# Kernel tuning notes

Hardware: AMD Instinct MI355X
Metric: run time of the kernel (lower is better)

## Reference

```python
import jax, jax.numpy as jnp
import numpy as np

REG = 0.1          # entropic regularization, as in the module
N_ITERS = 100      # fixed Sinkhorn iteration count (POT numItermax capped; see notes)


def _sqdist(x, y):
    # ot.dist default: squared Euclidean pairwise distances, [n, m]
    x2 = jnp.sum(x * x, axis=1)[:, None]
    y2 = jnp.sum(y * y, axis=1)[None, :]
    M = x2 + y2 - 2.0 * (x @ y.T)
    return jnp.maximum(M, 0.0)


def setup_inputs() -> dict:
    key = jax.random.key(0)
    kx, ky = jax.random.split(key)
    n, m, d = 4096, 4096, 32
    # uniform in [0, 0.5) keeps exp(-M/reg) representable in fp32
    x = jax.random.uniform(kx, (n, d), dtype=jnp.float32) * 0.5
    y = jax.random.uniform(ky, (m, d), dtype=jnp.float32) * 0.5
    return {"x": x, "y": y}


def reference(x, y):
    n, m = x.shape[0], y.shape[0]
    a = jnp.full((n,), 1.0 / n, dtype=x.dtype)   # uniform source marginal
    b = jnp.full((m,), 1.0 / m, dtype=y.dtype)   # uniform target marginal
    M = _sqdist(x, y)                            # [n, m] cost
    K = jnp.exp(-M / REG)                        # [n, m] Gibbs kernel

    u0 = jnp.full((n,), 1.0 / n, dtype=x.dtype)
    v0 = jnp.full((m,), 1.0 / m, dtype=y.dtype)

    def step(carry, _):
        u, v = carry
        u = a / (K @ v)      # [n]
        v = b / (K.T @ u)    # [m]
        return (u, v), None

    (u, v), _ = jax.lax.scan(step, (u0, v0), None, length=N_ITERS)
    # transport plan gamma = diag(u) K diag(v), as returned by ot.bregman.sinkhorn
    gamma = u[:, None] * K * v[None, :]
    return gamma
```

## Files before the change

kernel.cpp:

```cpp
#include <hip/hip_runtime.h>
#include <hip/hip_fp16.h>


#define NN 4096
#define MM 4096
#define DD 32
#define N_ITERS 100

static constexpr float INV_REG = 10.0f;
static constexpr float A_MARG  = 1.0f / 4096.0f;
static constexpr float B_MARG  = 1.0f / 4096.0f;

typedef _Float16 h2_t __attribute__((ext_vector_type(2)));
typedef unsigned u32v4 __attribute__((ext_vector_type(4)));

static __device__ __forceinline__ float dot2(unsigned a, unsigned b, float acc) {
#if __has_builtin(__builtin_amdgcn_fdot2)
    return __builtin_amdgcn_fdot2(__builtin_bit_cast(h2_t, a),
                                  __builtin_bit_cast(h2_t, b), acc, false);
#else
    float2 fa = __half22float2(*(const __half2*)&a);
    float2 fb = __half22float2(*(const __half2*)&b);
    acc = fmaf(fa.x, fb.x, acc);
    return fmaf(fa.y, fb.y, acc);
#endif
}

static __device__ __forceinline__ uint4 ld_nt_u4(const uint4* p) {
#if __has_builtin(__builtin_nontemporal_load)
    u32v4 r = __builtin_nontemporal_load((const u32v4*)p);
    uint4 o; o.x = r[0]; o.y = r[1]; o.z = r[2]; o.w = r[3];
    return o;
#else
    return *p;
#endif
}

static __device__ __forceinline__ unsigned ld_dev_u32(const unsigned* p) {
    return __hip_atomic_load(p, __ATOMIC_RELAXED, __HIP_MEMORY_SCOPE_AGENT);
}
static __device__ __forceinline__ void st_dev_u32(unsigned* p, unsigned v) {
    __hip_atomic_store(p, v, __ATOMIC_RELAXED, __HIP_MEMORY_SCOPE_AGENT);
}
static __device__ __forceinline__ unsigned short ld_dev_u16(const unsigned short* p) {
    return __hip_atomic_load(p, __ATOMIC_RELAXED, __HIP_MEMORY_SCOPE_AGENT);
}
static __device__ __forceinline__ void st_dev_u16(unsigned short* p, unsigned short v) {
    __hip_atomic_store(p, v, __ATOMIC_RELAXED, __HIP_MEMORY_SCOPE_AGENT);
}
static __device__ __forceinline__ unsigned long long ld_dev_u64(const unsigned long long* p) {
    return __hip_atomic_load(p, __ATOMIC_RELAXED, __HIP_MEMORY_SCOPE_AGENT);
}
static __device__ __forceinline__ void st_dev_u64(unsigned long long* p, unsigned long long v) {
    __hip_atomic_store(p, v, __ATOMIC_RELAXED, __HIP_MEMORY_SCOPE_AGENT);
}

__global__ void compute_K_half(const float* __restrict__ p, const float* __restrict__ q,
                               __half* __restrict__ Kh, __half* __restrict__ v16,
                               unsigned* __restrict__ conv, unsigned* __restrict__ slot,
                               unsigned* __restrict__ mtu, unsigned* __restrict__ mtv,
                               int prime) {
    const int tid = threadIdx.x;
    const int j   = blockIdx.x * 256 + tid;
    const int r0  = blockIdx.y * 16;

    if (prime && blockIdx.y == 0) {
        v16[j] = __float2half(B_MARG);
        if (blockIdx.x == 0) {
            if (tid == 0) { *conv = 0u; *slot = 1u; }
            mtu[tid] = 0u; mtu[tid + 256] = 0u;
            mtv[tid] = 0u; mtv[tid + 256] = 0u;
        }
    }

    float qv[DD];
    const float4* q4 = (const float4*)(q + (size_t)j * DD);
#pragma unroll
    for (int k = 0; k < DD / 4; ++k) {
        float4 t = q4[k];
        qv[4 * k + 0] = t.x; qv[4 * k + 1] = t.y;
        qv[4 * k + 2] = t.z; qv[4 * k + 3] = t.w;
    }

    __shared__ float ps[16 * DD];
    ps[tid]       = p[(size_t)r0 * DD + tid];
    ps[tid + 256] = p[(size_t)r0 * DD + tid + 256];
    __syncthreads();

#pragma unroll 4
    for (int ii = 0; ii < 16; ++ii) {
        float acc = 0.0f;
#pragma unroll
        for (int k = 0; k < DD; ++k) {
            float d = ps[ii * DD + k] - qv[k];
            acc = fmaf(d, d, acc);
        }
        Kh[(size_t)(r0 + ii) * MM + j] = __float2half(__expf(-acc * INV_REG));
    }
}

__global__ void __launch_bounds__(1024, 8)
sinkhorn_persist(const __half* __restrict__ Kh, const __half* __restrict__ KTh,
                 float* __restrict__ u32g, float* __restrict__ v32g,
                 unsigned short* __restrict__ hist,
                 unsigned* __restrict__ mtu, unsigned* __restrict__ mtv,
                 unsigned long long* __restrict__ mdu,
                 unsigned long long* __restrict__ mdv) {
    __shared__ __align__(16) __half vlds[MM];
    __shared__ float part[16];
    __shared__ unsigned fb_lds[8];
    const int tid  = threadIdx.x;
    const int lane = tid & 63;
    const int w    = tid >> 6;
    const int rib  = w >> 1;
    const int hlf  = w & 1;
    const int bid  = blockIdx.x;
    const int i    = bid * 8 + rib;
    const int g0   = hlf * 256 + lane;
    const uint4* __restrict__ MU = (const uint4*)(Kh  + (size_t)i * MM);
    const uint4* __restrict__ MV = (const uint4*)(KTh + (size_t)i * MM);

    uint4 k0 = MU[g0], k1 = MU[g0 + 64], k2 = MU[g0 + 128], k3 = MU[g0 + 192];

    for (int t = 0; t < N_ITERS; ++t) {
        if (t == 0) {
            if (tid < 512) {
                const unsigned long long dv =
                    (unsigned long long)__half_as_ushort(__float2half(B_MARG)) *
                    0x0001000100010001ULL;
                ((unsigned long long*)vlds)[2 * tid]     = dv;
                ((unsigned long long*)vlds)[2 * tid + 1] = dv;
            }
            __syncthreads();
        } else {
            if (tid < 512) {
                const unsigned want = 2u * (unsigned)t;
                unsigned tg;
                for (;;) {
                    tg = ld_dev_u32(mtv + tid);
                    if ((tg & 0x7fffffffu) == want) break;
                    __builtin_amdgcn_s_sleep(1);
                }
                asm volatile("" ::: "memory");
                unsigned long long d0 = ld_dev_u64(mdv + 2 * tid);
                unsigned long long d1 = ld_dev_u64(mdv + 2 * tid + 1);
                ((unsigned long long*)vlds)[2 * tid]     = d0;
                ((unsigned long long*)vlds)[2 * tid + 1] = d1;
                const bool allf = __all((tg >> 31) != 0u);
                if ((tid & 63) == 0) fb_lds[tid >> 6] = allf ? 1u : 0u;
            }
            __syncthreads();
            if ((t & 1) == 0) {
                if ((fb_lds[0] & fb_lds[1] & fb_lds[2] & fb_lds[3] &
                     fb_lds[4] & fb_lds[5] & fb_lds[6] & fb_lds[7]) != 0u)
                    break;
            }
        }

        {
            const uint4* V = (const uint4*)vlds;
            const uint4 a = V[g0], b = V[g0 + 64], c = V[g0 + 128], d = V[g0 + 192];
            float x0 = 0.f, x1 = 0.f, x2 = 0.f, x3 = 0.f;
            x0 = dot2(k0.x, a.x, x0); x0 = dot2(k0.y, a.y, x0);
            x0 = dot2(k0.z, a.z, x0); x0 = dot2(k0.w, a.w, x0);
            x1 = dot2(k1.x, b.x, x1); x1 = dot2(k1.y, b.y, x1);
            x1 = dot2(k1.z, b.z, x1); x1 = dot2(k1.w, b.w, x1);
            x2 = dot2(k2.x, c.x, x2); x2 = dot2(k2.y, c.y, x2);
            x2 = dot2(k2.z, c.z, x2); x2 = dot2(k2.w, c.w, x2);
            x3 = dot2(k3.x, d.x, x3); x3 = dot2(k3.y, d.y, x3);
            x3 = dot2(k3.z, d.z, x3); x3 = dot2(k3.w, d.w, x3);
            float acc = (x0 + x1) + (x2 + x3);
#pragma unroll
            for (int off = 32; off > 0; off >>= 1) acc += __shfl_down(acc, off, 64);
            if (lane == 0) part[w] = acc;
        }
        if (w != 0) {
            k0 = ld_nt_u4(MV + g0);       k1 = ld_nt_u4(MV + g0 + 64);
            k2 = ld_nt_u4(MV + g0 + 128); k3 = ld_nt_u4(MV + g0 + 192);
        }
        __syncthreads();
        if (tid == 0) {
            unsigned long long d0 = 0, d1 = 0;
#pragma unroll
            for (int q = 0; q < 8; ++q) {
                float r = A_MARG / (part[2 * q] + part[2 * q + 1]);
                u32g[bid * 8 + q] = r;
                const unsigned long long h =
                    (unsigned long long)__half_as_ushort(__float2half(r));
                if (q < 4) d0 |= h << (16 * q); else d1 |= h << (16 * (q - 4));
            }
            st_dev_u64(mdu + 2 * bid,     d0);
            st_dev_u64(mdu + 2 * bid + 1, d1);
            asm volatile("s_waitcnt vmcnt(0)" ::: "memory");
            st_dev_u32(mtu + bid, 2u * (unsigned)t + 1u);
        }
        if (w == 0) {
            k0 = ld_nt_u4(MV + g0);       k1 = ld_nt_u4(MV + g0 + 64);
            k2 = ld_nt_u4(MV + g0 + 128); k3 = ld_nt_u4(MV + g0 + 192);
        }

        if (tid < 512) {
            const unsigned want = 2u * (unsigned)t + 1u;
            unsigned tg;
            for (;;) {
                tg = ld_dev_u32(mtu + tid);
                if ((tg & 0x7fffffffu) == want) break;
                __builtin_amdgcn_s_sleep(1);
            }
            asm volatile("" ::: "memory");
            unsigned long long d0 = ld_dev_u64(mdu + 2 * tid);
            unsigned long long d1 = ld_dev_u64(mdu + 2 * tid + 1);
            ((unsigned long long*)vlds)[2 * tid]     = d0;
            ((unsigned long long*)vlds)[2 * tid + 1] = d1;
        }
        __syncthreads();

        {
            const uint4* V = (const uint4*)vlds;
            const uint4 a = V[g0], b = V[g0 + 64], c = V[g0 + 128], d = V[g0 + 192];
            float x0 = 0.f, x1 = 0.f, x2 = 0.f, x3 = 0.f;
            x0 = dot2(k0.x, a.x, x0); x0 = dot2(k0.y, a.y, x0);
            x0 = dot2(k0.z, a.z, x0); x0 = dot2(k0.w, a.w, x0);
            x1 = dot2(k1.x, b.x, x1); x1 = dot2(k1.y, b.y, x1);
            x1 = dot2(k1.z, b.z, x1); x1 = dot2(k1.w, b.w, x1);
            x2 = dot2(k2.x, c.x, x2); x2 = dot2(k2.y, c.y, x2);
            x2 = dot2(k2.z, c.z, x2); x2 = dot2(k2.w, c.w, x2);
            x3 = dot2(k3.x, d.x, x3); x3 = dot2(k3.y, d.y, x3);
            x3 = dot2(k3.z, d.z, x3); x3 = dot2(k3.w, d.w, x3);
            float acc = (x0 + x1) + (x2 + x3);
#pragma unroll
            for (int off = 32; off > 0; off >>= 1) acc += __shfl_down(acc, off, 64);
            if (lane == 0) part[w] = acc;
        }
        if (w != 0) {
            k0 = MU[g0]; k1 = MU[g0 + 64]; k2 = MU[g0 + 128]; k3 = MU[g0 + 192];
        }
        __syncthreads();
        if (tid == 0) {
            unsigned long long d0 = 0, d1 = 0;
#pragma unroll
            for (int q = 0; q < 8; ++q) {
                float r = B_MARG / (part[2 * q] + part[2 * q + 1]);
                v32g[bid * 8 + q] = r;
                const unsigned long long h =
                    (unsigned long long)__half_as_ushort(__float2half(r));
                if (q < 4) d0 |= h << (16 * q); else d1 |= h << (16 * (q - 4));
            }
            unsigned tg = 2u * (unsigned)t + 2u;
            if (t & 1) {
                unsigned long long h0 = ld_dev_u64((unsigned long long*)hist + 2 * bid);
                unsigned long long h1 = ld_dev_u64((unsigned long long*)hist + 2 * bid + 1);
                if (h0 == d0 && h1 == d1) tg |= 0x80000000u;
                st_dev_u64((unsigned long long*)hist + 2 * bid,     d0);
                st_dev_u64((unsigned long long*)hist + 2 * bid + 1, d1);
            }
            st_dev_u64(mdv + 2 * bid,     d0);
            st_dev_u64(mdv + 2 * bid + 1, d1);
            asm volatile("s_waitcnt vmcnt(0)" ::: "memory");
            st_dev_u32(mtv + bid, tg);
        }
        if (w == 0) {
            k0 = MU[g0]; k1 = MU[g0 + 64]; k2 = MU[g0 + 128]; k3 = MU[g0 + 192];
        }
    }
}

__global__ void __launch_bounds__(1024, 8)
rowpass_u(const __half* __restrict__ Mat, const __half* __restrict__ w16_in,
          float* __restrict__ w32_out, __half* __restrict__ w16_out,
          unsigned* __restrict__ conv, unsigned* __restrict__ slot, int t) {
    if (ld_dev_u32(conv)) return;
    if ((t & 1) == 0) {
        if (ld_dev_u32(slot) == 0u) {
            if (threadIdx.x == 0) st_dev_u32(conv, 1u);
            return;
        }
    } else {
        if (blockIdx.x == 0 && threadIdx.x == 0) st_dev_u32(slot, 0u);
    }

    __shared__ __align__(16) __half vlds[MM];
    __shared__ float part[16];
    const int tid  = threadIdx.x;
    const int lane = tid & 63;
    const int w    = tid >> 6;
    const int rib  = w >> 1;
    const int hlf  = w & 1;
    const int i    = blockIdx.x * 8 + rib;
    const uint4* __restrict__ Mrow = (const uint4*)(Mat + (size_t)i * MM);
    const int g0 = hlf * 256 + lane;

    uint4 stg;
    if (tid < 512) stg = ((const uint4*)w16_in)[tid];
    const uint4 k0 = Mrow[g0];
    const uint4 k1 = Mrow[g0 + 64];
    const uint4 k2 = Mrow[g0 + 128];
    const uint4 k3 = Mrow[g0 + 192];
    if (tid < 512) ((uint4*)vlds)[tid] = stg;
    __syncthreads();

    const uint4* V = (const uint4*)vlds;
    const uint4 v0 = V[g0];
    const uint4 v1 = V[g0 + 64];
    const uint4 v2 = V[g0 + 128];
    const uint4 v3 = V[g0 + 192];

    float a0 = 0.f, a1 = 0.f, a2 = 0.f, a3 = 0.f;
    a0 = dot2(k0.x, v0.x, a0); a0 = dot2(k0.y, v0.y, a0);
    a0 = dot2(k0.z, v0.z, a0); a0 = dot2(k0.w, v0.w, a0);
    a1 = dot2(k1.x, v1.x, a1); a1 = dot2(k1.y, v1.y, a1);
    a1 = dot2(k1.z, v1.z, a1); a1 = dot2(k1.w, v1.w, a1);
    a2 = dot2(k2.x, v2.x, a2); a2 = dot2(k2.y, v2.y, a2);
    a2 = dot2(k2.z, v2.z, a2); a2 = dot2(k2.w, v2.w, a2);
    a3 = dot2(k3.x, v3.x, a3); a3 = dot2(k3.y, v3.y, a3);
    a3 = dot2(k3.z, v3.z, a3); a3 = dot2(k3.w, v3.w, a3);
    float acc = (a0 + a1) + (a2 + a3);

#pragma unroll
    for (int off = 32; off > 0; off >>= 1) acc += __shfl_down(acc, off, 64);
    if (lane == 0) part[w] = acc;
    __syncthreads();

    if (tid < 8) {
        const int row = blockIdx.x * 8 + tid;
        float r = A_MARG / (part[2 * tid] + part[2 * tid + 1]);
        w32_out[row] = r;
        w16_out[row] = __float2half(r);
    }
}

__global__ void __launch_bounds__(1024, 8)
rowpass_v(const __half* __restrict__ Mat, const __half* __restrict__ w16_in,
          float* __restrict__ w32_out, __half* __restrict__ w16_out,
          unsigned short* __restrict__ hist,
          unsigned* __restrict__ conv, unsigned* __restrict__ slot, int t) {
    if (ld_dev_u32(conv)) return;

    __shared__ __align__(16) __half vlds[MM];
    __shared__ float part[16];
    const int tid  = threadIdx.x;
    const int lane = tid & 63;
    const int w    = tid >> 6;
    const int rib  = w >> 1;
    const int hlf  = w & 1;
    const int i    = blockIdx.x * 8 + rib;
    const uint4* __restrict__ Mrow = (const uint4*)(Mat + (size_t)i * MM);
    const int g0 = hlf * 256 + lane;

    uint4 stg;
    if (tid < 512) stg = ((const uint4*)w16_in)[tid];
    const uint4 k0 = Mrow[g0];
    const uint4 k1 = Mrow[g0 + 64];
    const uint4 k2 = Mrow[g0 + 128];
    const uint4 k3 = Mrow[g0 + 192];
    if (tid < 512) ((uint4*)vlds)[tid] = stg;
    __syncthreads();

    const uint4* V = (const uint4*)vlds;
    const uint4 v0 = V[g0];
    const uint4 v1 = V[g0 + 64];
    const uint4 v2 = V[g0 + 128];
    const uint4 v3 = V[g0 + 192];

    float a0 = 0.f, a1 = 0.f, a2 = 0.f, a3 = 0.f;
    a0 = dot2(k0.x, v0.x, a0); a0 = dot2(k0.y, v0.y, a0);
    a0 = dot2(k0.z, v0.z, a0); a0 = dot2(k0.w, v0.w, a0);
    a1 = dot2(k1.x, v1.x, a1); a1 = dot2(k1.y, v1.y, a1);
    a1 = dot2(k1.z, v1.z, a1); a1 = dot2(k1.w, v1.w, a1);
    a2 = dot2(k2.x, v2.x, a2); a2 = dot2(k2.y, v2.y, a2);
    a2 = dot2(k2.z, v2.z, a2); a2 = dot2(k2.w, v2.w, a2);
    a3 = dot2(k3.x, v3.x, a3); a3 = dot2(k3.y, v3.y, a3);
    a3 = dot2(k3.z, v3.z, a3); a3 = dot2(k3.w, v3.w, a3);
    float acc = (a0 + a1) + (a2 + a3);

#pragma unroll
    for (int off = 32; off > 0; off >>= 1) acc += __shfl_down(acc, off, 64);
    if (lane == 0) part[w] = acc;
    __syncthreads();

    if (tid < 8) {
        const int row = blockIdx.x * 8 + tid;
        float r = B_MARG / (part[2 * tid] + part[2 * tid + 1]);
        w32_out[row] = r;
        const __half h = __float2half(r);
        if (t & 1) {
            const unsigned short bits = __half_as_ushort(h);
            const unsigned short old2 = ld_dev_u16(hist + row);
            if (old2 != bits) st_dev_u32(slot, 1u);
            st_dev_u16(hist + row, bits);
        }
        w16_out[row] = h;
    }
}

__global__ void epilogue(const float* __restrict__ x, const float* __restrict__ y,
                         const float* __restrict__ u, const float* __restrict__ v,
                         float* __restrict__ out) {
    const int tid = threadIdx.x;
    const int j   = blockIdx.x * 256 + tid;
    const int r0  = blockIdx.y * 16;

    float yv[DD];
    const float4* y4 = (const float4*)(y + (size_t)j * DD);
#pragma unroll
    for (int k = 0; k < DD / 4; ++k) {
        float4 t = y4[k];
        yv[4 * k + 0] = t.x; yv[4 * k + 1] = t.y;
        yv[4 * k + 2] = t.z; yv[4 * k + 3] = t.w;
    }

    __shared__ float xs[16 * DD];
    __shared__ float u_lds[16];
    xs[tid]       = x[(size_t)r0 * DD + tid];
    xs[tid + 256] = x[(size_t)r0 * DD + tid + 256];
    if (tid < 16) u_lds[tid] = u[r0 + tid];
    __syncthreads();

    const float vj = v[j];
#pragma unroll 4
    for (int ii = 0; ii < 16; ++ii) {
        float acc = 0.0f;
#pragma unroll
        for (int k = 0; k < DD; ++k) {
            float d = xs[ii * DD + k] - yv[k];
            acc = fmaf(d, d, acc);
        }
        out[(size_t)(r0 + ii) * MM + j] = u_lds[ii] * __expf(-acc * INV_REG) * vj;
    }
}

extern "C" void kernel_launch(void* const* d_in, const int* in_sizes, int n_in,
                              void* d_out, int out_size, void* d_ws, size_t ws_size,
                              hipStream_t stream) {
    const float* x = (const float*)d_in[0];
    const float* y = (const float*)d_in[1];
    __half*   Kh   = (__half*)d_ws;
    __half*   KTh  = Kh + (size_t)NN * MM;
    float*    u32  = (float*)(KTh + (size_t)NN * MM);
    float*    v32  = u32 + NN;
    __half*   u16  = (__half*)(v32 + MM);
    __half*   v16  = u16 + NN;
    unsigned short* hist = (unsigned short*)(v16 + MM);
    unsigned* slot = (unsigned*)(hist + MM);
    unsigned* conv = slot + 1;
    unsigned* mtu  = slot + 512;
    unsigned* mtv  = mtu + 512;
    unsigned long long* mdu = (unsigned long long*)(mtv + 512);
    unsigned long long* mdv = mdu + 1024;
    float*    out  = (float*)d_out;

    compute_K_half<<<dim3(MM / 256, NN / 16), 256, 0, stream>>>(x, y, Kh, v16, conv, slot, mtu, mtv, 1);
    compute_K_half<<<dim3(NN / 256, MM / 16), 256, 0, stream>>>(y, x, KTh, v16, conv, slot, mtu, mtv, 0);

    {
        void* args[] = { &Kh, &KTh, &u32, &v32, &hist, &mtu, &mtv, &mdu, &mdv };
        hipError_t e = hipLaunchCooperativeKernel((const void*)sinkhorn_persist,
                                                  dim3(512), dim3(1024), args, 0, stream);
        if (e != hipSuccess) {
            (void)hipGetLastError();
            for (int t = 0; t < N_ITERS; ++t) {
                rowpass_u<<<NN / 8, 1024, 0, stream>>>(Kh,  v16, u32, u16, conv, slot, t);
                rowpass_v<<<MM / 8, 1024, 0, stream>>>(KTh, u16, v32, v16, hist, conv, slot, t);
            }
        }
    }

    epilogue<<<dim3(MM / 256, NN / 16), 256, 0, stream>>>(x, y, u32, v32, out);
}
```

Baseline: 621.4 us.

## Load broadcast vectors directly into registers per wave, drop LDS staging barriers

```diff
diff --git a/kernel.cpp b/kernel.cpp
--- a/kernel.cpp
+++ b/kernel.cpp
@@ -55,6 +55,15 @@
     __hip_atomic_store(p, v, __ATOMIC_RELAXED, __HIP_MEMORY_SCOPE_AGENT);
 }
 
+static __device__ __forceinline__ uint4 ld_ent(const unsigned long long* md, int e) {
+    unsigned long long d0 = ld_dev_u64(md + 2 * e);
+    unsigned long long d1 = ld_dev_u64(md + 2 * e + 1);
+    uint4 r;
+    r.x = (unsigned)d0; r.y = (unsigned)(d0 >> 32);
+    r.z = (unsigned)d1; r.w = (unsigned)(d1 >> 32);
+    return r;
+}
+
 __global__ void compute_K_half(const float* __restrict__ p, const float* __restrict__ q,
                                __half* __restrict__ Kh, __half* __restrict__ v16,
                                unsigned* __restrict__ conv, unsigned* __restrict__ slot,
@@ -102,13 +111,11 @@
 __global__ void __launch_bounds__(1024, 8)
 sinkhorn_persist(const __half* __restrict__ Kh, const __half* __restrict__ KTh,
                  float* __restrict__ u32g, float* __restrict__ v32g,
-                 unsigned short* __restrict__ hist,
                  unsigned* __restrict__ mtu, unsigned* __restrict__ mtv,
                  unsigned long long* __restrict__ mdu,
                  unsigned long long* __restrict__ mdv) {
-    __shared__ __align__(16) __half vlds[MM];
     __shared__ float part[16];
-    __shared__ unsigned fb_lds[8];
+    __shared__ unsigned fb_lds[16];
     const int tid  = threadIdx.x;
     const int lane = tid & 63;
     const int w    = tid >> 6;
@@ -117,58 +124,48 @@
     const int bid  = blockIdx.x;
     const int i    = bid * 8 + rib;
     const int g0   = hlf * 256 + lane;
+    const int e0 = g0, e1 = g0 + 64, e2 = g0 + 128, e3 = g0 + 192;
     const uint4* __restrict__ MU = (const uint4*)(Kh  + (size_t)i * MM);
     const uint4* __restrict__ MV = (const uint4*)(KTh + (size_t)i * MM);
 
+    unsigned long long h0p = ~0ULL, h1p = ~0ULL;
+
     uint4 k0 = MU[g0], k1 = MU[g0 + 64], k2 = MU[g0 + 128], k3 = MU[g0 + 192];
 
     for (int t = 0; t < N_ITERS; ++t) {
+        uint4 va, vb, vc, vd;
         if (t == 0) {
-            if (tid < 512) {
-                const unsigned long long dv =
-                    (unsigned long long)__half_as_ushort(__float2half(B_MARG)) *
-                    0x0001000100010001ULL;
-                ((unsigned long long*)vlds)[2 * tid]     = dv;
-                ((unsigned long long*)vlds)[2 * tid + 1] = dv;
-            }
-            __syncthreads();
+            const unsigned dv2 =
+                0x00010001u * (unsigned)__half_as_ushort(__float2half(B_MARG));
+            va.x = va.y = va.z = va.w = dv2; vb = va; vc = va; vd = va;
         } else {
-            if (tid < 512) {
-                const unsigned want = 2u * (unsigned)t;
-                unsigned tg;
-                for (;;) {
-                    tg = ld_dev_u32(mtv + tid);
-                    if ((tg & 0x7fffffffu) == want) break;
-                    __builtin_amdgcn_s_sleep(1);
-                }
-                asm volatile("" ::: "memory");
-                unsigned long long d0 = ld_dev_u64(mdv + 2 * tid);
-                unsigned long long d1 = ld_dev_u64(mdv + 2 * tid + 1);
-                ((unsigned long long*)vlds)[2 * tid]     = d0;
-                ((unsigned long long*)vlds)[2 * tid + 1] = d1;
-                const bool allf = __all((tg >> 31) != 0u);
-                if ((tid & 63) == 0) fb_lds[tid >> 6] = allf ? 1u : 0u;
-            }
-            __syncthreads();
-            if ((t & 1) == 0) {
-                if ((fb_lds[0] & fb_lds[1] & fb_lds[2] & fb_lds[3] &
-                     fb_lds[4] & fb_lds[5] & fb_lds[6] & fb_lds[7]) != 0u)
+            const unsigned want = 2u * (unsigned)t;
+            unsigned t0, t1, t2, t3;
+            for (;;) {
+                t0 = ld_dev_u32(mtv + e0); t1 = ld_dev_u32(mtv + e1);
+                t2 = ld_dev_u32(mtv + e2); t3 = ld_dev_u32(mtv + e3);
+                if (((t0 & 0x7fffffffu) == want) && ((t1 & 0x7fffffffu) == want) &&
+                    ((t2 & 0x7fffffffu) == want) && ((t3 & 0x7fffffffu) == want))
                     break;
-            }
+                __builtin_amdgcn_s_sleep(1);
+            }
+            asm volatile("" ::: "memory");
+            va = ld_ent(mdv, e0); vb = ld_ent(mdv, e1);
+            vc = ld_ent(mdv, e2); vd = ld_ent(mdv, e3);
+            const bool fz = __all(((t0 & t1 & t2 & t3) >> 31) != 0u);
+            if (lane == 0) fb_lds[w] = fz ? 1u : 0u;
         }
 
         {
-            const uint4* V = (const uint4*)vlds;
-            const uint4 a = V[g0], b = V[g0 + 64], c = V[g0 + 128], d = V[g0 + 192];
             float x0 = 0.f, x1 = 0.f, x2 = 0.f, x3 = 0.f;
-            x0 = dot2(k0.x, a.x, x0); x0 = dot2(k0.y, a.y, x0);
-            x0 = dot2(k0.z, a.z, x0); x0 = dot2(k0.w, a.w, x0);
-            x1 = dot2(k1.x, b.x, x1); x1 = dot2(k1.y, b.y, x1);
-            x1 = dot2(k1.z, b.z, x1); x1 = dot2(k1.w, b.w, x1);
-            x2 = dot2(k2.x, c.x, x2); x2 = dot2(k2.y, c.y, x2);
-            x2 = dot2(k2.z, c.z, x2); x2 = dot2(k2.w, c.w, x2);
-            x3 = dot2(k3.x, d.x, x3); x3 = dot2(k3.y, d.y, x3);
-            x3 = dot2(k3.z, d.z, x3); x3 = dot2(k3.w, d.w, x3);
+            x0 = dot2(k0.x, va.x, x0); x0 = dot2(k0.y, va.y, x0);
+            x0 = dot2(k0.z, va.z, x0); x0 = dot2(k0.w, va.w, x0);
+            x1 = dot2(k1.x, vb.x, x1); x1 = dot2(k1.y, vb.y, x1);
+            x1 = dot2(k1.z, vb.z, x1); x1 = dot2(k1.w, vb.w, x1);
+            x2 = dot2(k2.x, vc.x, x2); x2 = dot2(k2.y, vc.y, x2);
+            x2 = dot2(k2.z, vc.z, x2); x2 = dot2(k2.w, vc.w, x2);
+            x3 = dot2(k3.x, vd.x, x3); x3 = dot2(k3.y, vd.y, x3);
+            x3 = dot2(k3.z, vd.z, x3); x3 = dot2(k3.w, vd.w, x3);
             float acc = (x0 + x1) + (x2 + x3);
 #pragma unroll
             for (int off = 32; off > 0; off >>= 1) acc += __shfl_down(acc, off, 64);
@@ -179,54 +176,67 @@
             k2 = ld_nt_u4(MV + g0 + 128); k3 = ld_nt_u4(MV + g0 + 192);
         }
         __syncthreads();
-        if (tid == 0) {
-            unsigned long long d0 = 0, d1 = 0;
-#pragma unroll
-            for (int q = 0; q < 8; ++q) {
-                float r = A_MARG / (part[2 * q] + part[2 * q + 1]);
-                u32g[bid * 8 + q] = r;
-                const unsigned long long h =
-                    (unsigned long long)__half_as_ushort(__float2half(r));
-                if (q < 4) d0 |= h << (16 * q); else d1 |= h << (16 * (q - 4));
-            }
-            st_dev_u64(mdu + 2 * bid,     d0);
-            st_dev_u64(mdu + 2 * bid + 1, d1);
-            asm volatile("s_waitcnt vmcnt(0)" ::: "memory");
-            st_dev_u32(mtu + bid, 2u * (unsigned)t + 1u);
+        if (t != 0 && (t & 1) == 0) {
+            unsigned f = 1u;
+#pragma unroll
+            for (int q = 0; q < 16; ++q) f &= fb_lds[q];
+            if (f) break;
+        }
+        if (w == 0) {
+            unsigned hb = 0u;
+            if (lane < 8) {
+                float r = A_MARG / (part[2 * lane] + part[2 * lane + 1]);
+                u32g[bid * 8 + lane] = r;
+                hb = (unsigned)__half_as_ushort(__float2half(r));
+            }
+            const unsigned q0 = __shfl(hb, 0, 64), q1 = __shfl(hb, 1, 64);
+            const unsigned q2 = __shfl(hb, 2, 64), q3 = __shfl(hb, 3, 64);
+            const unsigned q4 = __shfl(hb, 4, 64), q5 = __shfl(hb, 5, 64);
+            const unsigned q6 = __shfl(hb, 6, 64), q7 = __shfl(hb, 7, 64);
+            if (lane == 0) {
+                const unsigned long long d0 =
+                    (unsigned long long)(q0 | (q1 << 16)) |
+                    ((unsigned long long)(q2 | (q3 << 16)) << 32);
+                const unsigned long long d1 =
+                    (unsigned long long)(q4 | (q5 << 16)) |
+                    ((unsigned long long)(q6 | (q7 << 16)) << 32);
+                st_dev_u64(mdu + 2 * bid,     d0);
+                st_dev_u64(mdu + 2 * bid + 1, d1);
+                asm volatile("s_waitcnt vmcnt(0)" ::: "memory");
+                st_dev_u32(mtu + bid, 2u * (unsigned)t + 1u);
+            }
         }
         if (w == 0) {
             k0 = ld_nt_u4(MV + g0);       k1 = ld_nt_u4(MV + g0 + 64);
             k2 = ld_nt_u4(MV + g0 + 128); k3 = ld_nt_u4(MV + g0 + 192);
         }
 
-        if (tid < 512) {
+        {
             const unsigned want = 2u * (unsigned)t + 1u;
-            unsigned tg;
+            unsigned t0, t1, t2, t3;
             for (;;) {
-                tg = ld_dev_u32(mtu + tid);
-                if ((tg & 0x7fffffffu) == want) break;
+                t0 = ld_dev_u32(mtu + e0); t1 = ld_dev_u32(mtu + e1);
+                t2 = ld_dev_u32(mtu + e2); t3 = ld_dev_u32(mtu + e3);
+                if (((t0 & 0x7fffffffu) == want) && ((t1 & 0x7fffffffu) == want) &&
+                    ((t2 & 0x7fffffffu) == want) && ((t3 & 0x7fffffffu) == want))
+                    break;
                 __builtin_amdgcn_s_sleep(1);
             }
             asm volatile("" ::: "memory");
-            unsigned long long d0 = ld_dev_u64(mdu + 2 * tid);
-            unsigned long long d1 = ld_dev_u64(mdu + 2 * tid + 1);
-            ((unsigned long long*)vlds)[2 * tid]     = d0;
-            ((unsigned long long*)vlds)[2 * tid + 1] = d1;
-        }
-        __syncthreads();
+            va = ld_ent(mdu, e0); vb = ld_ent(mdu, e1);
+            vc = ld_ent(mdu, e2); vd = ld_ent(mdu, e3);
+        }
 
         {
-            const uint4* V = (const uint4*)vlds;
-            const uint4 a = V[g0], b = V[g0 + 64], c = V[g0 + 128], d = V[g0 + 192];
             float x0 = 0.f, x1 = 0.f, x2 = 0.f, x3 = 0.f;
-            x0 = dot2(k0.x, a.x, x0); x0 = dot2(k0.y, a.y, x0);
-            x0 = dot2(k0.z, a.z, x0); x0 = dot2(k0.w, a.w, x0);
-            x1 = dot2(k1.x, b.x, x1); x1 = dot2(k1.y, b.y, x1);
-            x1 = dot2(k1.z, b.z, x1); x1 = dot2(k1.w, b.w, x1);
-            x2 = dot2(k2.x, c.x, x2); x2 = dot2(k2.y, c.y, x2);
-            x2 = dot2(k2.z, c.z, x2); x2 = dot2(k2.w, c.w, x2);
-            x3 = dot2(k3.x, d.x, x3); x3 = dot2(k3.y, d.y, x3);
-            x3 = dot2(k3.z, d.z, x3); x3 = dot2(k3.w, d.w, x3);
+            x0 = dot2(k0.x, va.x, x0); x0 = dot2(k0.y, va.y, x0);
+            x0 = dot2(k0.z, va.z, x0); x0 = dot2(k0.w, va.w, x0);
+            x1 = dot2(k1.x, vb.x, x1); x1 = dot2(k1.y, vb.y, x1);
+            x1 = dot2(k1.z, vb.z, x1); x1 = dot2(k1.w, vb.w, x1);
+            x2 = dot2(k2.x, vc.x, x2); x2 = dot2(k2.y, vc.y, x2);
+            x2 = dot2(k2.z, vc.z, x2); x2 = dot2(k2.w, vc.w, x2);
+            x3 = dot2(k3.x, vd.x, x3); x3 = dot2(k3.y, vd.y, x3);
+            x3 = dot2(k3.z, vd.z, x3); x3 = dot2(k3.w, vd.w, x3);
             float acc = (x0 + x1) + (x2 + x3);
 #pragma unroll
             for (int off = 32; off > 0; off >>= 1) acc += __shfl_down(acc, off, 64);
@@ -236,28 +246,34 @@
             k0 = MU[g0]; k1 = MU[g0 + 64]; k2 = MU[g0 + 128]; k3 = MU[g0 + 192];
         }
         __syncthreads();
-        if (tid == 0) {
-            unsigned long long d0 = 0, d1 = 0;
-#pragma unroll
-            for (int q = 0; q < 8; ++q) {
-                float r = B_MARG / (part[2 * q] + part[2 * q + 1]);
-                v32g[bid * 8 + q] = r;
-                const unsigned long long h =
-                    (unsigned long long)__half_as_ushort(__float2half(r));
-                if (q < 4) d0 |= h << (16 * q); else d1 |= h << (16 * (q - 4));
-            }
-            unsigned tg = 2u * (unsigned)t + 2u;
-            if (t & 1) {
-                unsigned long long h0 = ld_dev_u64((unsigned long long*)hist + 2 * bid);
-                unsigned long long h1 = ld_dev_u64((unsigned long long*)hist + 2 * bid + 1);
-                if (h0 == d0 && h1 == d1) tg |= 0x80000000u;
-                st_dev_u64((unsigned long long*)hist + 2 * bid,     d0);
-                st_dev_u64((unsigned long long*)hist + 2 * bid + 1, d1);
-            }
-            st_dev_u64(mdv + 2 * bid,     d0);
-            st_dev_u64(mdv + 2 * bid + 1, d1);
-            asm volatile("s_waitcnt vmcnt(0)" ::: "memory");
-            st_dev_u32(mtv + bid, tg);
+        if (w == 0) {
+            unsigned hb = 0u;
+            if (lane < 8) {
+                float r = B_MARG / (part[2 * lane] + part[2 * lane + 1]);
+                v32g[bid * 8 + lane] = r;
+                hb = (unsigned)__half_as_ushort(__float2half(r));
+            }
+            const unsigned q0 = __shfl(hb, 0, 64), q1 = __shfl(hb, 1, 64);
+            const unsigned q2 = __shfl(hb, 2, 64), q3 = __shfl(hb, 3, 64);
+            const unsigned q4 = __shfl(hb, 4, 64), q5 = __shfl(hb, 5, 64);
+            const unsigned q6 = __shfl(hb, 6, 64), q7 = __shfl(hb, 7, 64);
+            if (lane == 0) {
+                const unsigned long long d0 =
+                    (unsigned long long)(q0 | (q1 << 16)) |
+                    ((unsigned long long)(q2 | (q3 << 16)) << 32);
+                const unsigned long long d1 =
+                    (unsigned long long)(q4 | (q5 << 16)) |
+                    ((unsigned long long)(q6 | (q7 << 16)) << 32);
+                unsigned tg = 2u * (unsigned)t + 2u;
+                if (t & 1) {
+                    if (d0 == h0p && d1 == h1p) tg |= 0x80000000u;
+                    h0p = d0; h1p = d1;
+                }
+                st_dev_u64(mdv + 2 * bid,     d0);
+                st_dev_u64(mdv + 2 * bid + 1, d1);
+                asm volatile("s_waitcnt vmcnt(0)" ::: "memory");
+                st_dev_u32(mtv + bid, tg);
+            }
         }
         if (w == 0) {
             k0 = MU[g0]; k1 = MU[g0 + 64]; k2 = MU[g0 + 128]; k3 = MU[g0 + 192];
@@ -453,7 +469,7 @@
     compute_K_half<<<dim3(NN / 256, MM / 16), 256, 0, stream>>>(y, x, KTh, v16, conv, slot, mtu, mtv, 0);
 
     {
-        void* args[] = { &Kh, &KTh, &u32, &v32, &hist, &mtu, &mtv, &mdu, &mdv };
+        void* args[] = { &Kh, &KTh, &u32, &v32, &mtu, &mtv, &mdu, &mdv };
         hipError_t e = hipLaunchCooperativeKernel((const void*)sinkhorn_persist,
                                                   dim3(512), dim3(1024), args, 0, stream);
         if (e != hipSuccess) {
```

Measured after the change: 1.016 ms. 63.6% more time.

## Keep both K and K^T row slices resident in registers across Sinkhorn iterations

Applied to the files above, without the earlier changes.

```diff
diff --git a/kernel.cpp b/kernel.cpp
--- a/kernel.cpp
+++ b/kernel.cpp
@@ -12,7 +12,6 @@
 static constexpr float B_MARG  = 1.0f / 4096.0f;
 
 typedef _Float16 h2_t __attribute__((ext_vector_type(2)));
-typedef unsigned u32v4 __attribute__((ext_vector_type(4)));
 
 static __device__ __forceinline__ float dot2(unsigned a, unsigned b, float acc) {
 #if __has_builtin(__builtin_amdgcn_fdot2)
@@ -26,16 +25,6 @@
 #endif
 }
 
-static __device__ __forceinline__ uint4 ld_nt_u4(const uint4* p) {
-#if __has_builtin(__builtin_nontemporal_load)
-    u32v4 r = __builtin_nontemporal_load((const u32v4*)p);
-    uint4 o; o.x = r[0]; o.y = r[1]; o.z = r[2]; o.w = r[3];
-    return o;
-#else
-    return *p;
-#endif
-}
-
 static __device__ __forceinline__ unsigned ld_dev_u32(const unsigned* p) {
     return __hip_atomic_load(p, __ATOMIC_RELAXED, __HIP_MEMORY_SCOPE_AGENT);
 }
@@ -102,7 +91,6 @@
 __global__ void __launch_bounds__(1024, 8)
 sinkhorn_persist(const __half* __restrict__ Kh, const __half* __restrict__ KTh,
                  float* __restrict__ u32g, float* __restrict__ v32g,
-                 unsigned short* __restrict__ hist,
                  unsigned* __restrict__ mtu, unsigned* __restrict__ mtv,
                  unsigned long long* __restrict__ mdu,
                  unsigned long long* __restrict__ mdv) {
@@ -120,7 +108,10 @@
     const uint4* __restrict__ MU = (const uint4*)(Kh  + (size_t)i * MM);
     const uint4* __restrict__ MV = (const uint4*)(KTh + (size_t)i * MM);
 
-    uint4 k0 = MU[g0], k1 = MU[g0 + 64], k2 = MU[g0 + 128], k3 = MU[g0 + 192];
+    const uint4 ku0 = MU[g0], ku1 = MU[g0 + 64], ku2 = MU[g0 + 128], ku3 = MU[g0 + 192];
+    const uint4 kv0 = MV[g0], kv1 = MV[g0 + 64], kv2 = MV[g0 + 128], kv3 = MV[g0 + 192];
+
+    unsigned long long h0p = ~0ULL, h1p = ~0ULL;
 
     for (int t = 0; t < N_ITERS; ++t) {
         if (t == 0) {
@@ -161,42 +152,43 @@
             const uint4* V = (const uint4*)vlds;
             const uint4 a = V[g0], b = V[g0 + 64], c = V[g0 + 128], d = V[g0 + 192];
             float x0 = 0.f, x1 = 0.f, x2 = 0.f, x3 = 0.f;
-            x0 = dot2(k0.x, a.x, x0); x0 = dot2(k0.y, a.y, x0);
-            x0 = dot2(k0.z, a.z, x0); x0 = dot2(k0.w, a.w, x0);
-            x1 = dot2(k1.x, b.x, x1); x1 = dot2(k1.y, b.y, x1);
-            x1 = dot2(k1.z, b.z, x1); x1 = dot2(k1.w, b.w, x1);
-            x2 = dot2(k2.x, c.x, x2); x2 = dot2(k2.y, c.y, x2);
-            x2 = dot2(k2.z, c.z, x2); x2 = dot2(k2.w, c.w, x2);
-            x3 = dot2(k3.x, d.x, x3); x3 = dot2(k3.y, d.y, x3);
-            x3 = dot2(k3.z, d.z, x3); x3 = dot2(k3.w, d.w, x3);
+            x0 = dot2(ku0.x, a.x, x0); x0 = dot2(ku0.y, a.y, x0);
+            x0 = dot2(ku0.z, a.z, x0); x0 = dot2(ku0.w, a.w, x0);
+            x1 = dot2(ku1.x, b.x, x1); x1 = dot2(ku1.y, b.y, x1);
+            x1 = dot2(ku1.z, b.z, x1); x1 = dot2(ku1.w, b.w, x1);
+            x2 = dot2(ku2.x, c.x, x2); x2 = dot2(ku2.y, c.y, x2);
+            x2 = dot2(ku2.z, c.z, x2); x2 = dot2(ku2.w, c.w, x2);
+            x3 = dot2(ku3.x, d.x, x3); x3 = dot2(ku3.y, d.y, x3);
+            x3 = dot2(ku3.z, d.z, x3); x3 = dot2(ku3.w, d.w, x3);
             float acc = (x0 + x1) + (x2 + x3);
 #pragma unroll
             for (int off = 32; off > 0; off >>= 1) acc += __shfl_down(acc, off, 64);
             if (lane == 0) part[w] = acc;
         }
-        if (w != 0) {
-            k0 = ld_nt_u4(MV + g0);       k1 = ld_nt_u4(MV + g0 + 64);
-            k2 = ld_nt_u4(MV + g0 + 128); k3 = ld_nt_u4(MV + g0 + 192);
-        }
         __syncthreads();
-        if (tid == 0) {
-            unsigned long long d0 = 0, d1 = 0;
-#pragma unroll
-            for (int q = 0; q < 8; ++q) {
-                float r = A_MARG / (part[2 * q] + part[2 * q + 1]);
-                u32g[bid * 8 + q] = r;
-                const unsigned long long h =
-                    (unsigned long long)__half_as_ushort(__float2half(r));
-                if (q < 4) d0 |= h << (16 * q); else d1 |= h << (16 * (q - 4));
-            }
-            st_dev_u64(mdu + 2 * bid,     d0);
-            st_dev_u64(mdu + 2 * bid + 1, d1);
-            asm volatile("s_waitcnt vmcnt(0)" ::: "memory");
-            st_dev_u32(mtu + bid, 2u * (unsigned)t + 1u);
-        }
         if (w == 0) {
-            k0 = ld_nt_u4(MV + g0);       k1 = ld_nt_u4(MV + g0 + 64);
-            k2 = ld_nt_u4(MV + g0 + 128); k3 = ld_nt_u4(MV + g0 + 192);
+            unsigned hb = 0u;
+            if (lane < 8) {
+                float r = A_MARG / (part[2 * lane] + part[2 * lane + 1]);
+                u32g[bid * 8 + lane] = r;
+                hb = (unsigned)__half_as_ushort(__float2half(r));
+            }
+            const unsigned q0 = __shfl(hb, 0, 64), q1 = __shfl(hb, 1, 64);
+            const unsigned q2 = __shfl(hb, 2, 64), q3 = __shfl(hb, 3, 64);
+            const unsigned q4 = __shfl(hb, 4, 64), q5 = __shfl(hb, 5, 64);
+            const unsigned q6 = __shfl(hb, 6, 64), q7 = __shfl(hb, 7, 64);
+            if (lane == 0) {
+                const unsigned long long d0 =
+                    (unsigned long long)(q0 | (q1 << 16)) |
+                    ((unsigned long long)(q2 | (q3 << 16)) << 32);
+                const unsigned long long d1 =
+                    (unsigned long long)(q4 | (q5 << 16)) |
+                    ((unsigned long long)(q6 | (q7 << 16)) << 32);
+                st_dev_u64(mdu + 2 * bid,     d0);
+                st_dev_u64(mdu + 2 * bid + 1, d1);
+                asm volatile("s_waitcnt vmcnt(0)" ::: "memory");
+                st_dev_u32(mtu + bid, 2u * (unsigned)t + 1u);
+            }
         }
 
         if (tid < 512) {
@@ -219,48 +211,48 @@
             const uint4* V = (const uint4*)vlds;
             const uint4 a = V[g0], b = V[g0 + 64], c = V[g0 + 128], d = V[g0 + 192];
             float x0 = 0.f, x1 = 0.f, x2 = 0.f, x3 = 0.f;
-            x0 = dot2(k0.x, a.x, x0); x0 = dot2(k0.y, a.y, x0);
-            x0 = dot2(k0.z, a.z, x0); x0 = dot2(k0.w, a.w, x0);
-            x1 = dot2(k1.x, b.x, x1); x1 = dot2(k1.y, b.y, x1);
-            x1 = dot2(k1.z, b.z, x1); x1 = dot2(k1.w, b.w, x1);
-            x2 = dot2(k2.x, c.x, x2); x2 = dot2(k2.y, c.y, x2);
-            x2 = dot2(k2.z, c.z, x2); x2 = dot2(k2.w, c.w, x2);
-            x3 = dot2(k3.x, d.x, x3); x3 = dot2(k3.y, d.y, x3);
-            x3 = dot2(k3.z, d.z, x3); x3 = dot2(k3.w, d.w, x3);
+            x0 = dot2(kv0.x, a.x, x0); x0 = dot2(kv0.y, a.y, x0);
+            x0 = dot2(kv0.z, a.z, x0); x0 = dot2(kv0.w, a.w, x0);
+            x1 = dot2(kv1.x, b.x, x1); x1 = dot2(kv1.y, b.y, x1);
+            x1 = dot2(kv1.z, b.z, x1); x1 = dot2(kv1.w, b.w, x1);
+            x2 = dot2(kv2.x, c.x, x2); x2 = dot2(kv2.y, c.y, x2);
+            x2 = dot2(kv2.z, c.z, x2); x2 = dot2(kv2.w, c.w, x2);
+            x3 = dot2(kv3.x, d.x, x3); x3 = dot2(kv3.y, d.y, x3);
+            x3 = dot2(kv3.z, d.z, x3); x3 = dot2(kv3.w, d.w, x3);
             float acc = (x0 + x1) + (x2 + x3);
 #pragma unroll
             for (int off = 32; off > 0; off >>= 1) acc += __shfl_down(acc, off, 64);
             if (lane == 0) part[w] = acc;
         }
-        if (w != 0) {
-            k0 = MU[g0]; k1 = MU[g0 + 64]; k2 = MU[g0 + 128]; k3 = MU[g0 + 192];
-        }
         __syncthreads();
-        if (tid == 0) {
-            unsigned long long d0 = 0, d1 = 0;
-#pragma unroll
-            for (int q = 0; q < 8; ++q) {
-                float r = B_MARG / (part[2 * q] + part[2 * q + 1]);
-                v32g[bid * 8 + q] = r;
-                const unsigned long long h =
-                    (unsigned long long)__half_as_ushort(__float2half(r));
-                if (q < 4) d0 |= h << (16 * q); else d1 |= h << (16 * (q - 4));
-            }
-            unsigned tg = 2u * (unsigned)t + 2u;
-            if (t & 1) {
-                unsigned long long h0 = ld_dev_u64((unsigned long long*)hist + 2 * bid);
-                unsigned long long h1 = ld_dev_u64((unsigned long long*)hist + 2 * bid + 1);
-                if (h0 == d0 && h1 == d1) tg |= 0x80000000u;
-                st_dev_u64((unsigned long long*)hist + 2 * bid,     d0);
-                st_dev_u64((unsigned long long*)hist + 2 * bid + 1, d1);
-            }
-            st_dev_u64(mdv + 2 * bid,     d0);
-            st_dev_u64(mdv + 2 * bid + 1, d1);
-            asm volatile("s_waitcnt vmcnt(0)" ::: "memory");
-            st_dev_u32(mtv + bid, tg);
-        }
         if (w == 0) {
-            k0 = MU[g0]; k1 = MU[g0 + 64]; k2 = MU[g0 + 128]; k3 = MU[g0 + 192];
+            unsigned hb = 0u;
+            if (lane < 8) {
+                float r = B_MARG / (part[2 * lane] + part[2 * lane + 1]);
+                v32g[bid * 8 + lane] = r;
+                hb = (unsigned)__half_as_ushort(__float2half(r));
+            }
+            const unsigned q0 = __shfl(hb, 0, 64), q1 = __shfl(hb, 1, 64);
+            const unsigned q2 = __shfl(hb, 2, 64), q3 = __shfl(hb, 3, 64);
+            const unsigned q4 = __shfl(hb, 4, 64), q5 = __shfl(hb, 5, 64);
+            const unsigned q6 = __shfl(hb, 6, 64), q7 = __shfl(hb, 7, 64);
+            if (lane == 0) {
+                const unsigned long long d0 =
+                    (unsigned long long)(q0 | (q1 << 16)) |
+                    ((unsigned long long)(q2 | (q3 << 16)) << 32);
+                const unsigned long long d1 =
+                    (unsigned long long)(q4 | (q5 << 16)) |
+                    ((unsigned long long)(q6 | (q7 << 16)) << 32);
+                unsigned tg = 2u * (unsigned)t + 2u;
+                if (t & 1) {
+                    if (d0 == h0p && d1 == h1p) tg |= 0x80000000u;
+                    h0p = d0; h1p = d1;
+                }
+                st_dev_u64(mdv + 2 * bid,     d0);
+                st_dev_u64(mdv + 2 * bid + 1, d1);
+                asm volatile("s_waitcnt vmcnt(0)" ::: "memory");
+                st_dev_u32(mtv + bid, tg);
+            }
         }
     }
 }
@@ -453,7 +445,7 @@
     compute_K_half<<<dim3(NN / 256, MM / 16), 256, 0, stream>>>(y, x, KTh, v16, conv, slot, mtu, mtv, 0);
 
     {
-        void* args[] = { &Kh, &KTh, &u32, &v32, &hist, &mtu, &mtv, &mdu, &mdv };
+        void* args[] = { &Kh, &KTh, &u32, &v32, &mtu, &mtv, &mdu, &mdv };
         hipError_t e = hipLaunchCooperativeKernel((const void*)sinkhorn_persist,
                                                   dim3(512), dim3(1024), args, 0, stream);
         if (e != hipSuccess) {
```

Result: no change. 614.5 us (-1.1%).
